# Optimization experiments

Hardware: AMD Instinct MI355X
Metric: run time of the kernel (lower is better)

Reference implementation:

```python
import jax, jax.numpy as jnp
import numpy as np

D_MODEL = 1024
N_HEADS = 16
HEAD_DIM = D_MODEL // N_HEADS  # 64
N_T = max(1, int(N_HEADS * 0.25))  # 4 time heads
N_S = N_HEADS - N_T               # 12 space heads
T_DIM = N_T * HEAD_DIM
S_DIM = N_S * HEAD_DIM
B, L = 2, 2048


def setup_inputs() -> dict:
    key = jax.random.key(0)
    ks = jax.random.split(key, 8)
    std = 0.02
    return {
        "x": jax.random.normal(ks[0], (B, L, D_MODEL), dtype=jnp.float32),
        "attention_mask": jnp.zeros((B, 1, 1, L), dtype=jnp.float32),
        # torch nn.Linear weights have shape (out_features, in_features)
        "w_qt": jax.random.normal(ks[1], (T_DIM, D_MODEL), dtype=jnp.float32) * std,
        "w_kt": jax.random.normal(ks[2], (T_DIM, D_MODEL), dtype=jnp.float32) * std,
        "w_qs": jax.random.normal(ks[3], (S_DIM, D_MODEL), dtype=jnp.float32) * std,
        "w_ks": jax.random.normal(ks[4], (S_DIM, D_MODEL), dtype=jnp.float32) * std,
        "w_sigma": jnp.zeros((1,), dtype=jnp.float32),
        "w_v": jax.random.normal(ks[5], (D_MODEL, D_MODEL), dtype=jnp.float32) * std,
        "w_o": jax.random.normal(ks[6], (D_MODEL, D_MODEL), dtype=jnp.float32) * std,
    }


def _heads(x, w, n_h):
    # x:(B,L,D) @ w.T:(D,out) -> (B,L,n_h,d_h) -> (B,n_h,L,d_h)
    b, l, _ = x.shape
    y = jnp.einsum('bld,td->blt', x, w)
    return y.reshape(b, l, n_h, HEAD_DIM).transpose(0, 2, 1, 3)


def reference(x, attention_mask, w_qt, w_kt, w_qs, w_ks, w_sigma, w_v, w_o):
    b, l, _ = x.shape
    scale = np.sqrt(HEAD_DIM).astype(np.float32)
    # F3: time heads (sign-flipped, scaled by learnable sigma) + space heads
    Qt = _heads(x, w_qt, N_T)
    Kt = _heads(x, w_kt, N_T)
    Qs = _heads(x, w_qs, N_S)
    Ks = _heads(x, w_ks, N_S)
    st = jnp.einsum('bhqd,bhkd->bhqk', Qt, Kt)  # (B,N_T,L,L)
    ss = jnp.einsum('bhqd,bhkd->bhqk', Qs, Ks)  # (B,N_S,L,L)
    sigma = jax.nn.sigmoid(w_sigma[0])
    score = jnp.concatenate([-sigma * st, ss], axis=1) / scale  # (B,H,L,L)
    score = score + attention_mask.astype(score.dtype)
    attn_probs = jax.nn.softmax(score, axis=-1).astype(x.dtype)
    # dropout p=0.0 -> identity
    V = _heads(x, w_v, N_HEADS)  # (B,H,L,d_h)
    out = jnp.einsum('bhqk,bhkd->bhqd', attn_probs, V)
    out = out.transpose(0, 2, 1, 3).reshape(b, l, D_MODEL)
    out = jnp.einsum('bld,od->blo', out, w_o)
    return out, attn_probs
```

## Files before the change

### kernel.cpp

```cpp
#include <hip/hip_runtime.h>

typedef __bf16 bf16x8 __attribute__((ext_vector_type(8)));
typedef float f32x4 __attribute__((ext_vector_type(4)));
typedef float f32x16 __attribute__((ext_vector_type(16)));
typedef short short4v __attribute__((ext_vector_type(4)));
typedef unsigned short ushort8 __attribute__((ext_vector_type(8)));
typedef unsigned int uint4v __attribute__((ext_vector_type(4)));

#define AS1 __attribute__((address_space(1)))
#define AS3 __attribute__((address_space(3)))
#define GLL16(g, l) __builtin_amdgcn_global_load_lds((const AS1 void*)(g), (AS3 void*)(l), 16, 0, 0)
#define MFMA16(a, b, c) __builtin_amdgcn_mfma_f32_16x16x32_bf16((a), (b), (c), 0, 0, 0)
#define MFMA32(a, b, c) __builtin_amdgcn_mfma_f32_32x32x16_bf16((a), (b), (c), 0, 0, 0)
#define WAITVM(N) asm volatile("s_waitcnt vmcnt(" #N ")" ::: "memory")
#define WAITLGKM0 asm volatile("s_waitcnt lgkmcnt(0)" ::: "memory")
#define L2E 1.44269504f

__device__ __forceinline__ unsigned short f2bf(float f) {
  unsigned int u = __builtin_bit_cast(unsigned int, f);
  u = (u + 0x7fffu + ((u >> 16) & 1u)) >> 16;
  return (unsigned short)u;
}

__device__ __forceinline__ unsigned int cvtpk_bf16(float lo, float hi) {
  unsigned int r;
  asm("v_cvt_pk_bf16_f32 %0, %1, %2" : "=v"(r) : "v"(lo), "v"(hi));
  return r;
}

__global__ void convert_kernel(const float* __restrict__ x,
                               const float* __restrict__ w_qt, const float* __restrict__ w_kt,
                               const float* __restrict__ w_qs, const float* __restrict__ w_ks,
                               const float* __restrict__ w_v, const float* __restrict__ w_o,
                               unsigned short* __restrict__ xb, unsigned short* __restrict__ wcat,
                               unsigned short* __restrict__ wob) {
  const int NX = 4096 * 1024, NW = 3072 * 1024, NO = 1024 * 1024;
  int stride = gridDim.x * blockDim.x;
  for (int i = blockIdx.x * blockDim.x + threadIdx.x; i < NX + NW + NO; i += stride) {
    if (i < NX) {
      xb[i] = f2bf(x[i]);
    } else if (i < NX + NW) {
      int j = i - NX;
      int n = j >> 10, k = j & 1023;
      const float* src;
      if (n < 256)        src = w_qt + n * 1024;
      else if (n < 1024)  src = w_qs + (n - 256) * 1024;
      else if (n < 1280)  src = w_kt + (n - 1024) * 1024;
      else if (n < 2048)  src = w_ks + (n - 1280) * 1024;
      else                src = w_v + (n - 2048) * 1024;
      wcat[j] = f2bf(src[k]);
    } else {
      int j = i - NX - NW;
      wob[j] = f2bf(w_o[j]);
    }
  }
}

__global__ __launch_bounds__(256) void gemm_qkv(const unsigned short* __restrict__ A,
                                                const unsigned short* __restrict__ Bw,
                                                unsigned short* __restrict__ qb,
                                                unsigned short* __restrict__ kb,
                                                unsigned short* __restrict__ vt) {
  __shared__ unsigned short As[128 * 32];
  __shared__ unsigned short Bs[128 * 32];
  const int t = threadIdx.x;
  const int lane = t & 63, wid = t >> 6;
  const int wm = wid >> 1, wn = wid & 1;
  const int lr = lane & 15, lg = lane >> 4;
  const int m0 = blockIdx.x * 128, n0 = blockIdx.y * 128;
  const int K = 1024;
  f32x4 acc[4][4] = {};
  const unsigned short* gA0 = A + (m0 + (t >> 2)) * K + (t & 3) * 8;
  const unsigned short* gB0 = Bw + (n0 + (t >> 2)) * K + (t & 3) * 8;
  char* lA = (char*)As + wid * 1024;
  char* lB = (char*)Bs + wid * 1024;
  for (int k0 = 0; k0 < K; k0 += 32) {
    __syncthreads();
    GLL16(gA0 + k0, lA);
    GLL16(gA0 + 64 * K + k0, lA + 4096);
    GLL16(gB0 + k0, lB);
    GLL16(gB0 + 64 * K + k0, lB + 4096);
    __syncthreads();
    bf16x8 af[4], bfr[4];
#pragma unroll
    for (int i = 0; i < 4; ++i) {
      af[i] = *(const bf16x8*)&As[(wm * 64 + i * 16 + lr) * 32 + lg * 8];
      bfr[i] = *(const bf16x8*)&Bs[(wn * 64 + i * 16 + lr) * 32 + lg * 8];
    }
#pragma unroll
    for (int i = 0; i < 4; ++i)
#pragma unroll
      for (int j = 0; j < 4; ++j)
        acc[i][j] = MFMA16(af[i], bfr[j], acc[i][j]);
  }
#pragma unroll
  for (int i = 0; i < 4; ++i) {
#pragma unroll
    for (int j = 0; j < 4; ++j) {
      int n = n0 + wn * 64 + j * 16 + lr;
      int mb = m0 + wm * 64 + i * 16 + lg * 4;
      f32x4 v = acc[i][j];
      if (n < 2048) {
        unsigned short* dst = (n < 1024) ? qb : kb;
        int nn = n & 1023;
        int h = nn >> 6, d = nn & 63;
#pragma unroll
        for (int r = 0; r < 4; ++r) {
          int m = mb + r;
          int b = m >> 11, l = m & 2047;
          dst[((b * 16 + h) * 2048 + l) * 64 + d] = f2bf(v[r]);
        }
      } else {
        int nn = n - 2048;
        int h = nn >> 6, d = nn & 63;
        int b = mb >> 11, l = mb & 2047;
        short4v pk;
        pk[0] = (short)f2bf(v[0]); pk[1] = (short)f2bf(v[1]);
        pk[2] = (short)f2bf(v[2]); pk[3] = (short)f2bf(v[3]);
        *(short4v*)&vt[((b * 16 + h) * 64 + d) * 2048 + l] = pk;
      }
    }
  }
}

__global__ __launch_bounds__(256, 3) void attn_kernel(const unsigned short* __restrict__ qb,
                                                      const unsigned short* __restrict__ kb,
                                                      const unsigned short* __restrict__ vt,
                                                      const float* __restrict__ mask,
                                                      const float* __restrict__ w_sigma,
                                                      float* __restrict__ probs,
                                                      unsigned short* __restrict__ ao) {
  __shared__ __align__(16) char smem[49792];
  const int t = threadIdx.x;
  const int lane = t & 63, w = t >> 6;
  const int col = lane & 31, hi = lane >> 5;
  const int srow = lane >> 3;
  const int schunk = (lane & 7) ^ (srow & 7);
  const int s = blockIdx.x;
  const int bh = (s & 7) * 4 + ((s >> 3) >> 6);
  const int q0 = ((s >> 3) & 63) * 32;
  const int b = bh >> 4, h = bh & 15;
  const float sigma = 1.0f / (1.0f + __expf(-w_sigma[0]));
  const float fac2 = ((h < 4) ? (-sigma * 0.125f) : 0.125f) * L2E;
  const float* maskb = mask + b * 2048;
  const int kbase = w * 512;

  char* Kl = smem + w * 4096;
  char* Vl = smem + 16384 + w * 4096;
  char* Pl = smem + 32768 + w * 4096;
  float (*psum)[32] = (float(*)[32])(smem + 49152);
  float* rsum = (float*)(smem + 49664);
  float* pvacc = (float*)smem;

  const unsigned short* kb_bh = kb + (size_t)bh * 2048 * 64;
  const unsigned short* vt_bh = vt + (size_t)bh * 64 * 2048;

  bf16x8 qf[4];
  {
    const unsigned short* qp = qb + (size_t)(bh * 2048 + q0 + col) * 64 + hi * 8;
#pragma unroll
    for (int m = 0; m < 4; ++m) qf[m] = *(const bf16x8*)(qp + m * 16);
  }

#pragma unroll
  for (int j = 0; j < 4; ++j)
    GLL16(kb_bh + (size_t)(kbase + j * 8 + srow) * 64 + schunk * 8, Kl + j * 1024);
  float rs[16];
#pragma unroll
  for (int r = 0; r < 16; ++r) rs[r] = 0.f;
  for (int c = 0; c < 16; ++c) {
    int kc = kbase + c * 32;
    char* curb = (c & 1) ? Vl : Kl;
    char* nxtb = (c & 1) ? Kl : Vl;
    if (c < 15) {
#pragma unroll
      for (int j = 0; j < 4; ++j)
        GLL16(kb_bh + (size_t)(kc + 32 + j * 8 + srow) * 64 + schunk * 8, nxtb + j * 1024);
      WAITVM(4);
    } else {
      WAITVM(0);
    }
    f32x16 sacc = {};
#pragma unroll
    for (int m = 0; m < 4; ++m) {
      bf16x8 kf = *(const bf16x8*)(curb + col * 128 + (((2 * m + hi) ^ (col & 7)) << 4));
      sacc = MFMA32(qf[m], kf, sacc);
    }
    float mv2 = maskb[kc + col] * L2E;
#pragma unroll
    for (int r = 0; r < 16; ++r) rs[r] += exp2f(sacc[r] * fac2 + mv2);
  }
#pragma unroll
  for (int o = 1; o < 32; o <<= 1)
#pragma unroll
    for (int r = 0; r < 16; ++r) rs[r] += __shfl_xor(rs[r], o);
  if (col == 0) {
#pragma unroll
    for (int r = 0; r < 16; ++r) psum[w][(r & 3) + 8 * (r >> 2) + 4 * hi] = rs[r];
  }
  __syncthreads();
  if (t < 32) rsum[t] = -log2f(psum[0][t] + psum[1][t] + psum[2][t] + psum[3][t]);
  __syncthreads();

  float rws_l[16];
#pragma unroll
  for (int r = 0; r < 16; ++r) rws_l[r] = rsum[(r & 3) + 8 * (r >> 2) + 4 * hi];

#pragma unroll
  for (int j = 0; j < 4; ++j)
    GLL16(kb_bh + (size_t)(kbase + j * 8 + srow) * 64 + schunk * 8, Kl + j * 1024);
#pragma unroll
  for (int j = 0; j < 4; ++j)
    GLL16(vt_bh + (size_t)(j * 8 + srow + (schunk >> 2) * 32) * 2048 + kbase + (schunk & 3) * 8,
          Vl + j * 1024);
  WAITVM(4);

  f32x16 oacc0 = {}, oacc1 = {};
  float* pp = probs + (size_t)(bh * 2048 + q0) * 2048;
  for (int c = 0; c < 16; ++c) {
    int kc = kbase + c * 32;
    WAITVM(8);
    f32x16 sacc = {};
#pragma unroll
    for (int m = 0; m < 4; ++m) {
      bf16x8 kf = *(const bf16x8*)(Kl + col * 128 + (((2 * m + hi) ^ (col & 7)) << 4));
      sacc = MFMA32(qf[m], kf, sacc);
    }
    WAITLGKM0;
    if (c < 15) {
#pragma unroll
      for (int j = 0; j < 4; ++j)
        GLL16(kb_bh + (size_t)(kc + 32 + j * 8 + srow) * 64 + schunk * 8, Kl + j * 1024);
    }
    float mv2 = maskb[kc + col] * L2E;
#pragma unroll
    for (int r = 0; r < 16; ++r) {
      float pv_ = exp2f(sacc[r] * fac2 + (rws_l[r] + mv2));
      int row = (r & 3) + 8 * (r >> 2) + 4 * hi;
      int off = (row * 128 + col * 4) ^ ((row & 7) << 4);
      *(float*)(Pl + off) = pv_;
    }
#pragma unroll
    for (int j2 = 0; j2 < 4; ++j2) {
      int row = j2 * 8 + srow;
      f32x4 v = *(const f32x4*)(Pl + row * 128 + (schunk << 4));
      __builtin_nontemporal_store(v, (f32x4*)(pp + (size_t)row * 2048 + kc + (lane & 7) * 4));
    }
    uint4v u0, u1;
#pragma unroll
    for (int kh = 0; kh < 2; ++kh) {
      int cbase = kh * 4 + hi * 2;
      f32x4 a0 = *(const f32x4*)(Pl + col * 128 + (((cbase + 0) ^ (col & 7)) << 4));
      f32x4 a1 = *(const f32x4*)(Pl + col * 128 + (((cbase + 1) ^ (col & 7)) << 4));
      uint4v u;
      u[0] = cvtpk_bf16(a0[0], a0[1]); u[1] = cvtpk_bf16(a0[2], a0[3]);
      u[2] = cvtpk_bf16(a1[0], a1[1]); u[3] = cvtpk_bf16(a1[2], a1[3]);
      if (kh == 0) u0 = u; else u1 = u;
    }
    if (c < 15) { WAITVM(8); } else { WAITVM(4); }
#pragma unroll
    for (int kh = 0; kh < 2; ++kh) {
      bf16x8 pa = __builtin_bit_cast(bf16x8, kh == 0 ? u0 : u1);
#pragma unroll
      for (int dh = 0; dh < 2; ++dh) {
        bf16x8 vf = *(const bf16x8*)(Vl + col * 128 + (((dh * 4 + kh * 2 + hi) ^ (col & 7)) << 4));
        if (dh == 0) oacc0 = MFMA32(pa, vf, oacc0);
        else         oacc1 = MFMA32(pa, vf, oacc1);
      }
    }
    WAITLGKM0;
    if (c < 15) {
#pragma unroll
      for (int j = 0; j < 4; ++j)
        GLL16(vt_bh + (size_t)(j * 8 + srow + (schunk >> 2) * 32) * 2048 + kc + 32 + (schunk & 3) * 8,
              Vl + j * 1024);
    }
  }

  __syncthreads();
  for (int i = t; i < 2048; i += 256) pvacc[i] = 0.0f;
  __syncthreads();
#pragma unroll
  for (int r = 0; r < 16; ++r) {
    int row = (r & 3) + 8 * (r >> 2) + 4 * hi;
    atomicAdd(&pvacc[row * 64 + col], oacc0[r]);
    atomicAdd(&pvacc[row * 64 + 32 + col], oacc1[r]);
  }
  __syncthreads();
  {
    int row = t >> 3, c8 = (t & 7) * 8;
    f32x4 v0 = *(const f32x4*)&pvacc[row * 64 + c8];
    f32x4 v1 = *(const f32x4*)&pvacc[row * 64 + c8 + 4];
    ushort8 o;
#pragma unroll
    for (int i = 0; i < 4; ++i) {
      o[i] = f2bf(v0[i]);
      o[i + 4] = f2bf(v1[i]);
    }
    *(ushort8*)&ao[((b * 2048) + q0 + row) * 1024 + h * 64 + c8] = o;
  }
}

__global__ __launch_bounds__(256) void gemm_oproj(const unsigned short* __restrict__ A,
                                                  const unsigned short* __restrict__ Bw,
                                                  float* __restrict__ out) {
  __shared__ unsigned short As[128 * 32];
  __shared__ unsigned short Bs[128 * 32];
  const int t = threadIdx.x;
  const int lane = t & 63, wid = t >> 6;
  const int wm = wid >> 1, wn = wid & 1;
  const int lr = lane & 15, lg = lane >> 4;
  const int m0 = blockIdx.x * 128, n0 = blockIdx.y * 128;
  const int K = 1024;
  f32x4 acc[4][4] = {};
  const unsigned short* gA0 = A + (m0 + (t >> 2)) * K + (t & 3) * 8;
  const unsigned short* gB0 = Bw + (n0 + (t >> 2)) * K + (t & 3) * 8;
  char* lA = (char*)As + wid * 1024;
  char* lB = (char*)Bs + wid * 1024;
  for (int k0 = 0; k0 < K; k0 += 32) {
    __syncthreads();
    GLL16(gA0 + k0, lA);
    GLL16(gA0 + 64 * K + k0, lA + 4096);
    GLL16(gB0 + k0, lB);
    GLL16(gB0 + 64 * K + k0, lB + 4096);
    __syncthreads();
    bf16x8 af[4], bfr[4];
#pragma unroll
    for (int i = 0; i < 4; ++i) {
      af[i] = *(const bf16x8*)&As[(wm * 64 + i * 16 + lr) * 32 + lg * 8];
      bfr[i] = *(const bf16x8*)&Bs[(wn * 64 + i * 16 + lr) * 32 + lg * 8];
    }
#pragma unroll
    for (int i = 0; i < 4; ++i)
#pragma unroll
      for (int j = 0; j < 4; ++j)
        acc[i][j] = MFMA16(af[i], bfr[j], acc[i][j]);
  }
#pragma unroll
  for (int i = 0; i < 4; ++i) {
#pragma unroll
    for (int j = 0; j < 4; ++j) {
      int n = n0 + wn * 64 + j * 16 + lr;
      int mb = m0 + wm * 64 + i * 16 + lg * 4;
#pragma unroll
      for (int r = 0; r < 4; ++r)
        out[(mb + r) * 1024 + n] = acc[i][j][r];
    }
  }
}

extern "C" void kernel_launch(void* const* d_in, const int* in_sizes, int n_in,
                              void* d_out, int out_size, void* d_ws, size_t ws_size,
                              hipStream_t stream) {
  const float* x       = (const float*)d_in[0];
  const float* amask   = (const float*)d_in[1];
  const float* w_qt    = (const float*)d_in[2];
  const float* w_kt    = (const float*)d_in[3];
  const float* w_qs    = (const float*)d_in[4];
  const float* w_ks    = (const float*)d_in[5];
  const float* w_sigma = (const float*)d_in[6];
  const float* w_v     = (const float*)d_in[7];
  const float* w_o     = (const float*)d_in[8];

  char* ws = (char*)d_ws;
  unsigned short* xb   = (unsigned short*)ws;
  unsigned short* wcat = (unsigned short*)(ws + 8388608);
  unsigned short* wob  = (unsigned short*)(ws + 14680064);
  unsigned short* qb   = (unsigned short*)(ws + 16777216);
  unsigned short* kb   = (unsigned short*)(ws + 25165824);
  unsigned short* vt   = (unsigned short*)(ws + 33554432);
  unsigned short* ao   = (unsigned short*)(ws + 41943040);

  float* outp = (float*)d_out;
  float* probs = outp + 4194304;

  convert_kernel<<<2048, 256, 0, stream>>>(x, w_qt, w_kt, w_qs, w_ks, w_v, w_o, xb, wcat, wob);
  gemm_qkv<<<dim3(32, 24), 256, 0, stream>>>(xb, wcat, qb, kb, vt);
  attn_kernel<<<2048, 256, 0, stream>>>(qb, kb, vt, amask, w_sigma, probs, ao);
  gemm_oproj<<<dim3(32, 8), 256, 0, stream>>>(ao, wob, outp);
}
```

Baseline: 310.6 us.

## Split attention into separate row-sum and main kernels with MFMA priority hints

The two-pass attention kernel becomes two launches. A lighter row-sum kernel with higher occupancy computes the softmax log-normalisers into a workspace buffer, and the main kernel reads them to write probabilities and compute PV. Mask values are preloaded into registers and s_setprio is raised around MFMA blocks. The split adds a kernel launch, a global round trip for the row sums, and recomputation of Q loads, in exchange for better occupancy in the first pass and less LDS in the main kernel.

```diff
diff --git a/kernel.cpp b/kernel.cpp
--- a/kernel.cpp
+++ b/kernel.cpp
@@ -123,14 +123,13 @@
   }
 }
 
-__global__ __launch_bounds__(256, 3) void attn_kernel(const unsigned short* __restrict__ qb,
+__global__ __launch_bounds__(256, 4) void attn_rowsum(const unsigned short* __restrict__ qb,
                                                       const unsigned short* __restrict__ kb,
-                                                      const unsigned short* __restrict__ vt,
                                                       const float* __restrict__ mask,
                                                       const float* __restrict__ w_sigma,
-                                                      float* __restrict__ probs,
-                                                      unsigned short* __restrict__ ao) {
-  __shared__ __align__(16) char smem[49792];
+                                                      float* __restrict__ rws) {
+  __shared__ __align__(16) char smemK[32768];
+  __shared__ float psum[4][32];
   const int t = threadIdx.x;
   const int lane = t & 63, w = t >> 6;
   const int col = lane & 31, hi = lane >> 5;
@@ -144,12 +143,91 @@
   const float fac2 = ((h < 4) ? (-sigma * 0.125f) : 0.125f) * L2E;
   const float* maskb = mask + b * 2048;
   const int kbase = w * 512;
+  char* Kbuf = smemK + w * 8192;
+
+  const unsigned short* kb_bh = kb + (size_t)bh * 2048 * 64;
+
+  bf16x8 qf[4];
+  {
+    const unsigned short* qp = qb + (size_t)(bh * 2048 + q0 + col) * 64 + hi * 8;
+#pragma unroll
+    for (int m = 0; m < 4; ++m) qf[m] = *(const bf16x8*)(qp + m * 16);
+  }
+  float mv2[16];
+#pragma unroll
+  for (int c = 0; c < 16; ++c) mv2[c] = maskb[kbase + c * 32 + col] * L2E;
+
+#pragma unroll
+  for (int j = 0; j < 4; ++j)
+    GLL16(kb_bh + (size_t)(kbase + j * 8 + srow) * 64 + schunk * 8, Kbuf + j * 1024);
+
+  float rs[16];
+#pragma unroll
+  for (int r = 0; r < 16; ++r) rs[r] = 0.f;
+  for (int c = 0; c < 16; ++c) {
+    int kc = kbase + c * 32;
+    if (c < 15) {
+      char* nb = Kbuf + ((c + 1) & 1) * 4096;
+#pragma unroll
+      for (int j = 0; j < 4; ++j)
+        GLL16(kb_bh + (size_t)(kc + 32 + j * 8 + srow) * 64 + schunk * 8, nb + j * 1024);
+      WAITVM(4);
+    } else {
+      WAITVM(0);
+    }
+    char* cb = Kbuf + (c & 1) * 4096;
+    __builtin_amdgcn_s_setprio(1);
+    f32x16 sacc = {};
+#pragma unroll
+    for (int m = 0; m < 4; ++m) {
+      bf16x8 kf = *(const bf16x8*)(cb + col * 128 + (((2 * m + hi) ^ (col & 7)) << 4));
+      sacc = MFMA32(qf[m], kf, sacc);
+    }
+    __builtin_amdgcn_s_setprio(0);
+#pragma unroll
+    for (int r = 0; r < 16; ++r) rs[r] += exp2f(sacc[r] * fac2 + mv2[c]);
+  }
+#pragma unroll
+  for (int o = 1; o < 32; o <<= 1)
+#pragma unroll
+    for (int r = 0; r < 16; ++r) rs[r] += __shfl_xor(rs[r], o);
+  if (col == 0) {
+#pragma unroll
+    for (int r = 0; r < 16; ++r) psum[w][(r & 3) + 8 * (r >> 2) + 4 * hi] = rs[r];
+  }
+  __syncthreads();
+  if (t < 32) {
+    float ssum = psum[0][t] + psum[1][t] + psum[2][t] + psum[3][t];
+    rws[bh * 2048 + q0 + t] = -log2f(ssum);
+  }
+}
+
+__global__ __launch_bounds__(256, 3) void attn_main(const unsigned short* __restrict__ qb,
+                                                    const unsigned short* __restrict__ kb,
+                                                    const unsigned short* __restrict__ vt,
+                                                    const float* __restrict__ mask,
+                                                    const float* __restrict__ w_sigma,
+                                                    const float* __restrict__ rws,
+                                                    float* __restrict__ probs,
+                                                    unsigned short* __restrict__ ao) {
+  __shared__ __align__(16) char smem[49152];
+  const int t = threadIdx.x;
+  const int lane = t & 63, w = t >> 6;
+  const int col = lane & 31, hi = lane >> 5;
+  const int srow = lane >> 3;
+  const int schunk = (lane & 7) ^ (srow & 7);
+  const int s = blockIdx.x;
+  const int bh = (s & 7) * 4 + ((s >> 3) >> 6);
+  const int q0 = ((s >> 3) & 63) * 32;
+  const int b = bh >> 4, h = bh & 15;
+  const float sigma = 1.0f / (1.0f + __expf(-w_sigma[0]));
+  const float fac2 = ((h < 4) ? (-sigma * 0.125f) : 0.125f) * L2E;
+  const float* maskb = mask + b * 2048;
+  const int kbase = w * 512;
 
   char* Kl = smem + w * 4096;
   char* Vl = smem + 16384 + w * 4096;
   char* Pl = smem + 32768 + w * 4096;
-  float (*psum)[32] = (float(*)[32])(smem + 49152);
-  float* rsum = (float*)(smem + 49664);
   float* pvacc = (float*)smem;
 
   const unsigned short* kb_bh = kb + (size_t)bh * 2048 * 64;
@@ -161,50 +239,15 @@
 #pragma unroll
     for (int m = 0; m < 4; ++m) qf[m] = *(const bf16x8*)(qp + m * 16);
   }
-
-#pragma unroll
-  for (int j = 0; j < 4; ++j)
-    GLL16(kb_bh + (size_t)(kbase + j * 8 + srow) * 64 + schunk * 8, Kl + j * 1024);
-  float rs[16];
-#pragma unroll
-  for (int r = 0; r < 16; ++r) rs[r] = 0.f;
-  for (int c = 0; c < 16; ++c) {
-    int kc = kbase + c * 32;
-    char* curb = (c & 1) ? Vl : Kl;
-    char* nxtb = (c & 1) ? Kl : Vl;
-    if (c < 15) {
-#pragma unroll
-      for (int j = 0; j < 4; ++j)
-        GLL16(kb_bh + (size_t)(kc + 32 + j * 8 + srow) * 64 + schunk * 8, nxtb + j * 1024);
-      WAITVM(4);
-    } else {
-      WAITVM(0);
-    }
-    f32x16 sacc = {};
-#pragma unroll
-    for (int m = 0; m < 4; ++m) {
-      bf16x8 kf = *(const bf16x8*)(curb + col * 128 + (((2 * m + hi) ^ (col & 7)) << 4));
-      sacc = MFMA32(qf[m], kf, sacc);
-    }
-    float mv2 = maskb[kc + col] * L2E;
-#pragma unroll
-    for (int r = 0; r < 16; ++r) rs[r] += exp2f(sacc[r] * fac2 + mv2);
-  }
-#pragma unroll
-  for (int o = 1; o < 32; o <<= 1)
-#pragma unroll
-    for (int r = 0; r < 16; ++r) rs[r] += __shfl_xor(rs[r], o);
-  if (col == 0) {
-#pragma unroll
-    for (int r = 0; r < 16; ++r) psum[w][(r & 3) + 8 * (r >> 2) + 4 * hi] = rs[r];
-  }
-  __syncthreads();
-  if (t < 32) rsum[t] = -log2f(psum[0][t] + psum[1][t] + psum[2][t] + psum[3][t]);
-  __syncthreads();
-
   float rws_l[16];
-#pragma unroll
-  for (int r = 0; r < 16; ++r) rws_l[r] = rsum[(r & 3) + 8 * (r >> 2) + 4 * hi];
+  {
+    const float* rwsb = rws + bh * 2048 + q0;
+#pragma unroll
+    for (int r = 0; r < 16; ++r) rws_l[r] = rwsb[(r & 3) + 8 * (r >> 2) + 4 * hi];
+  }
+  float mv2[16];
+#pragma unroll
+  for (int c = 0; c < 16; ++c) mv2[c] = maskb[kbase + c * 32 + col] * L2E;
 
 #pragma unroll
   for (int j = 0; j < 4; ++j)
@@ -219,23 +262,24 @@
   float* pp = probs + (size_t)(bh * 2048 + q0) * 2048;
   for (int c = 0; c < 16; ++c) {
     int kc = kbase + c * 32;
-    WAITVM(8);
+    if (c > 0) WAITVM(8);
+    __builtin_amdgcn_s_setprio(1);
     f32x16 sacc = {};
 #pragma unroll
     for (int m = 0; m < 4; ++m) {
       bf16x8 kf = *(const bf16x8*)(Kl + col * 128 + (((2 * m + hi) ^ (col & 7)) << 4));
       sacc = MFMA32(qf[m], kf, sacc);
     }
+    __builtin_amdgcn_s_setprio(0);
     WAITLGKM0;
     if (c < 15) {
 #pragma unroll
       for (int j = 0; j < 4; ++j)
         GLL16(kb_bh + (size_t)(kc + 32 + j * 8 + srow) * 64 + schunk * 8, Kl + j * 1024);
     }
-    float mv2 = maskb[kc + col] * L2E;
 #pragma unroll
     for (int r = 0; r < 16; ++r) {
-      float pv_ = exp2f(sacc[r] * fac2 + (rws_l[r] + mv2));
+      float pv_ = exp2f(sacc[r] * fac2 + (rws_l[r] + mv2[c]));
       int row = (r & 3) + 8 * (r >> 2) + 4 * hi;
       int off = (row * 128 + col * 4) ^ ((row & 7) << 4);
       *(float*)(Pl + off) = pv_;
@@ -258,6 +302,7 @@
       if (kh == 0) u0 = u; else u1 = u;
     }
     if (c < 15) { WAITVM(8); } else { WAITVM(4); }
+    __builtin_amdgcn_s_setprio(1);
 #pragma unroll
     for (int kh = 0; kh < 2; ++kh) {
       bf16x8 pa = __builtin_bit_cast(bf16x8, kh == 0 ? u0 : u1);
@@ -268,6 +313,7 @@
         else         oacc1 = MFMA32(pa, vf, oacc1);
       }
     }
+    __builtin_amdgcn_s_setprio(0);
     WAITLGKM0;
     if (c < 15) {
 #pragma unroll
@@ -370,12 +416,14 @@
   unsigned short* kb   = (unsigned short*)(ws + 25165824);
   unsigned short* vt   = (unsigned short*)(ws + 33554432);
   unsigned short* ao   = (unsigned short*)(ws + 41943040);
+  float* rws           = (float*)(ws + 50331648);
 
   float* outp = (float*)d_out;
   float* probs = outp + 4194304;
 
   convert_kernel<<<2048, 256, 0, stream>>>(x, w_qt, w_kt, w_qs, w_ks, w_v, w_o, xb, wcat, wob);
   gemm_qkv<<<dim3(32, 24), 256, 0, stream>>>(xb, wcat, qb, kb, vt);
-  attn_kernel<<<2048, 256, 0, stream>>>(qb, kb, vt, amask, w_sigma, probs, ao);
+  attn_rowsum<<<2048, 256, 0, stream>>>(qb, kb, amask, w_sigma, rws);
+  attn_main<<<2048, 256, 0, stream>>>(qb, kb, vt, amask, w_sigma, rws, probs, ao);
   gemm_oproj<<<dim3(32, 8), 256, 0, stream>>>(ao, wob, outp);
 }
```

Result: slower. 362.6 us (+16.7%).

## Keep attention probabilities in registers via transposed score MFMA and fold mask into V

Applied to the files above, without the earlier changes.

The P@V operand is now built directly in registers. A second, transposed QK^T MFMA is computed, exponentiated, and reshuffled with v_permlane32_swap, which replaces the LDS round-trip through a P staging buffer. The mask term is folded into V by scaling V with exp(mask) in the QKV GEMM epilogue, and probability stores now go straight from registers as scalar nontemporal stores. The softmax row-sum reduction is moved after the K/V prefetch is issued so it can overlap the loads. The cost is doubled QK MFMA work, a clamp on the exponent, and less vectorized global stores of probs, in exchange for less LDS traffic and smaller shared memory.

```diff
diff --git a/kernel.cpp b/kernel.cpp
--- a/kernel.cpp
+++ b/kernel.cpp
@@ -58,6 +58,7 @@
 
 __global__ __launch_bounds__(256) void gemm_qkv(const unsigned short* __restrict__ A,
                                                 const unsigned short* __restrict__ Bw,
+                                                const float* __restrict__ amask,
                                                 unsigned short* __restrict__ qb,
                                                 unsigned short* __restrict__ kb,
                                                 unsigned short* __restrict__ vt) {
@@ -114,9 +115,11 @@
         int nn = n - 2048;
         int h = nn >> 6, d = nn & 63;
         int b = mb >> 11, l = mb & 2047;
+        const float* mrow = amask + b * 2048 + l;
         short4v pk;
-        pk[0] = (short)f2bf(v[0]); pk[1] = (short)f2bf(v[1]);
-        pk[2] = (short)f2bf(v[2]); pk[3] = (short)f2bf(v[3]);
+#pragma unroll
+        for (int r = 0; r < 4; ++r)
+          pk[r] = (short)f2bf(v[r] * __expf(mrow[r]));
         *(short4v*)&vt[((b * 16 + h) * 64 + d) * 2048 + l] = pk;
       }
     }
@@ -130,7 +133,7 @@
                                                       const float* __restrict__ w_sigma,
                                                       float* __restrict__ probs,
                                                       unsigned short* __restrict__ ao) {
-  __shared__ __align__(16) char smem[49792];
+  __shared__ __align__(16) char smem[33408];
   const int t = threadIdx.x;
   const int lane = t & 63, w = t >> 6;
   const int col = lane & 31, hi = lane >> 5;
@@ -147,9 +150,8 @@
 
   char* Kl = smem + w * 4096;
   char* Vl = smem + 16384 + w * 4096;
-  char* Pl = smem + 32768 + w * 4096;
-  float (*psum)[32] = (float(*)[32])(smem + 49152);
-  float* rsum = (float*)(smem + 49664);
+  float (*psum)[32] = (float(*)[32])(smem + 32768);
+  float* rsum = (float*)(smem + 33280);
   float* pvacc = (float*)smem;
 
   const unsigned short* kb_bh = kb + (size_t)bh * 2048 * 64;
@@ -190,22 +192,7 @@
 #pragma unroll
     for (int r = 0; r < 16; ++r) rs[r] += exp2f(sacc[r] * fac2 + mv2);
   }
-#pragma unroll
-  for (int o = 1; o < 32; o <<= 1)
-#pragma unroll
-    for (int r = 0; r < 16; ++r) rs[r] += __shfl_xor(rs[r], o);
-  if (col == 0) {
-#pragma unroll
-    for (int r = 0; r < 16; ++r) psum[w][(r & 3) + 8 * (r >> 2) + 4 * hi] = rs[r];
-  }
-  __syncthreads();
-  if (t < 32) rsum[t] = -log2f(psum[0][t] + psum[1][t] + psum[2][t] + psum[3][t]);
-  __syncthreads();
-
-  float rws_l[16];
-#pragma unroll
-  for (int r = 0; r < 16; ++r) rws_l[r] = rsum[(r & 3) + 8 * (r >> 2) + 4 * hi];
-
+  WAITLGKM0;
 #pragma unroll
   for (int j = 0; j < 4; ++j)
     GLL16(kb_bh + (size_t)(kbase + j * 8 + srow) * 64 + schunk * 8, Kl + j * 1024);
@@ -213,18 +200,37 @@
   for (int j = 0; j < 4; ++j)
     GLL16(vt_bh + (size_t)(j * 8 + srow + (schunk >> 2) * 32) * 2048 + kbase + (schunk & 3) * 8,
           Vl + j * 1024);
-  WAITVM(4);
+#pragma unroll
+  for (int o = 1; o < 32; o <<= 1)
+#pragma unroll
+    for (int r = 0; r < 16; ++r) rs[r] += __shfl_xor(rs[r], o);
+  if (col == 0) {
+#pragma unroll
+    for (int r = 0; r < 16; ++r) psum[w][(r & 3) + 8 * (r >> 2) + 4 * hi] = rs[r];
+  }
+  __syncthreads();
+  if (t < 32) rsum[t] = -log2f(psum[0][t] + psum[1][t] + psum[2][t] + psum[3][t]);
+  __syncthreads();
+
+  float rws_l[16];
+#pragma unroll
+  for (int r = 0; r < 16; ++r) rws_l[r] = rsum[(r & 3) + 8 * (r >> 2) + 4 * hi];
+  const float rws_t = rsum[col];
 
   f32x16 oacc0 = {}, oacc1 = {};
   float* pp = probs + (size_t)(bh * 2048 + q0) * 2048;
   for (int c = 0; c < 16; ++c) {
     int kc = kbase + c * 32;
-    WAITVM(8);
-    f32x16 sacc = {};
+    if (c == 0) { WAITVM(4); } else { WAITVM(20); }
+    bf16x8 kf[4];
+#pragma unroll
+    for (int m = 0; m < 4; ++m)
+      kf[m] = *(const bf16x8*)(Kl + col * 128 + (((2 * m + hi) ^ (col & 7)) << 4));
+    f32x16 sn = {}, st_ = {};
 #pragma unroll
     for (int m = 0; m < 4; ++m) {
-      bf16x8 kf = *(const bf16x8*)(Kl + col * 128 + (((2 * m + hi) ^ (col & 7)) << 4));
-      sacc = MFMA32(qf[m], kf, sacc);
+      sn  = MFMA32(qf[m], kf[m], sn);
+      st_ = MFMA32(kf[m], qf[m], st_);
     }
     WAITLGKM0;
     if (c < 15) {
@@ -233,34 +239,28 @@
         GLL16(kb_bh + (size_t)(kc + 32 + j * 8 + srow) * 64 + schunk * 8, Kl + j * 1024);
     }
     float mv2 = maskb[kc + col] * L2E;
-#pragma unroll
-    for (int r = 0; r < 16; ++r) {
-      float pv_ = exp2f(sacc[r] * fac2 + (rws_l[r] + mv2));
-      int row = (r & 3) + 8 * (r >> 2) + 4 * hi;
-      int off = (row * 128 + col * 4) ^ ((row & 7) << 4);
-      *(float*)(Pl + off) = pv_;
-    }
-#pragma unroll
-    for (int j2 = 0; j2 < 4; ++j2) {
-      int row = j2 * 8 + srow;
-      f32x4 v = *(const f32x4*)(Pl + row * 128 + (schunk << 4));
-      __builtin_nontemporal_store(v, (f32x4*)(pp + (size_t)row * 2048 + kc + (lane & 7) * 4));
-    }
-    uint4v u0, u1;
+    float pn[16];
+#pragma unroll
+    for (int r = 0; r < 16; ++r) pn[r] = exp2f(sn[r] * fac2 + (rws_l[r] + mv2));
+    float pt[16];
+#pragma unroll
+    for (int r = 0; r < 16; ++r) pt[r] = exp2f(fminf(st_[r] * fac2 + rws_t, 60.0f));
+    unsigned int A0 = cvtpk_bf16(pt[0], pt[1]),  B0 = cvtpk_bf16(pt[4], pt[5]);
+    unsigned int C0 = cvtpk_bf16(pt[2], pt[3]),  D0 = cvtpk_bf16(pt[6], pt[7]);
+    unsigned int E0 = cvtpk_bf16(pt[8], pt[9]),  F0 = cvtpk_bf16(pt[12], pt[13]);
+    unsigned int G0 = cvtpk_bf16(pt[10], pt[11]), H0 = cvtpk_bf16(pt[14], pt[15]);
+    asm("v_permlane32_swap_b32 %0, %1" : "+v"(A0), "+v"(B0));
+    asm("v_permlane32_swap_b32 %0, %1" : "+v"(C0), "+v"(D0));
+    asm("v_permlane32_swap_b32 %0, %1" : "+v"(E0), "+v"(F0));
+    asm("v_permlane32_swap_b32 %0, %1" : "+v"(G0), "+v"(H0));
+    uint4v u1; u1[0] = A0; u1[1] = C0; u1[2] = B0; u1[3] = D0;
+    uint4v u2; u2[0] = E0; u2[1] = G0; u2[2] = F0; u2[3] = H0;
+    bf16x8 frag1 = __builtin_bit_cast(bf16x8, u1);
+    bf16x8 frag2 = __builtin_bit_cast(bf16x8, u2);
+    if (c == 0) { WAITVM(4); } else if (c < 15) { WAITVM(20); } else { WAITVM(16); }
 #pragma unroll
     for (int kh = 0; kh < 2; ++kh) {
-      int cbase = kh * 4 + hi * 2;
-      f32x4 a0 = *(const f32x4*)(Pl + col * 128 + (((cbase + 0) ^ (col & 7)) << 4));
-      f32x4 a1 = *(const f32x4*)(Pl + col * 128 + (((cbase + 1) ^ (col & 7)) << 4));
-      uint4v u;
-      u[0] = cvtpk_bf16(a0[0], a0[1]); u[1] = cvtpk_bf16(a0[2], a0[3]);
-      u[2] = cvtpk_bf16(a1[0], a1[1]); u[3] = cvtpk_bf16(a1[2], a1[3]);
-      if (kh == 0) u0 = u; else u1 = u;
-    }
-    if (c < 15) { WAITVM(8); } else { WAITVM(4); }
-#pragma unroll
-    for (int kh = 0; kh < 2; ++kh) {
-      bf16x8 pa = __builtin_bit_cast(bf16x8, kh == 0 ? u0 : u1);
+      bf16x8 pa = (kh == 0) ? frag1 : frag2;
 #pragma unroll
       for (int dh = 0; dh < 2; ++dh) {
         bf16x8 vf = *(const bf16x8*)(Vl + col * 128 + (((dh * 4 + kh * 2 + hi) ^ (col & 7)) << 4));
@@ -274,6 +274,12 @@
       for (int j = 0; j < 4; ++j)
         GLL16(vt_bh + (size_t)(j * 8 + srow + (schunk >> 2) * 32) * 2048 + kc + 32 + (schunk & 3) * 8,
               Vl + j * 1024);
+    }
+    float* pr = pp + kc + col;
+#pragma unroll
+    for (int r = 0; r < 16; ++r) {
+      int row = (r & 3) + 8 * (r >> 2) + 4 * hi;
+      __builtin_nontemporal_store(pn[r], pr + (size_t)row * 2048);
     }
   }
 
@@ -375,7 +381,7 @@
   float* probs = outp + 4194304;
 
   convert_kernel<<<2048, 256, 0, stream>>>(x, w_qt, w_kt, w_qs, w_ks, w_v, w_o, xb, wcat, wob);
-  gemm_qkv<<<dim3(32, 24), 256, 0, stream>>>(xb, wcat, qb, kb, vt);
+  gemm_qkv<<<dim3(32, 24), 256, 0, stream>>>(xb, wcat, amask, qb, kb, vt);
   attn_kernel<<<2048, 256, 0, stream>>>(qb, kb, vt, amask, w_sigma, probs, ao);
   gemm_oproj<<<dim3(32, 8), 256, 0, stream>>>(ao, wob, outp);
 }
```

Result: slower. 337.2 us (+8.6%).
